# Optimization experiments

Measured on AMD Instinct MI355X. Metric: run time of the kernel, lower is better.

Reference implementation:

```python
import jax, jax.numpy as jnp
import numpy as np

N_NODES = 32768


def setup_inputs() -> dict:
    key = jax.random.key(0)
    ks = jax.random.split(key, 6)
    x = jax.random.normal(ks[0], (N_NODES, 128), dtype=jnp.float32)
    edge_index = jax.random.randint(ks[1], (2, 262144), 0, N_NODES, dtype=jnp.int64)
    weights = jax.random.normal(ks[2], (64, 128, 128), dtype=jnp.float32) * (1.0 / np.sqrt(128.0))
    biases = jax.random.normal(ks[3], (64, 128), dtype=jnp.float32) * 0.02
    cls_w = jax.random.normal(ks[4], (128, 4), dtype=jnp.float32) * (1.0 / np.sqrt(128.0))
    cls_b = jax.random.normal(ks[5], (4,), dtype=jnp.float32) * 0.02
    return {"x": x, "edge_index": edge_index, "weights": weights,
            "biases": biases, "cls_w": cls_w, "cls_b": cls_b}


def reference(x, edge_index, weights, biases, cls_w, cls_b):
    n = x.shape[0]
    # GCN normalization with self-loops (PyG GCNConv default):
    # A_hat = D^-1/2 (A + I) D^-1/2, deg counted on target nodes.
    loop = jnp.arange(n, dtype=edge_index.dtype)
    src = jnp.concatenate([edge_index[0], loop])  # [E+N]
    dst = jnp.concatenate([edge_index[1], loop])  # [E+N]
    deg = jax.ops.segment_sum(jnp.ones_like(dst, dtype=x.dtype), dst, num_segments=n)
    dinv = jnp.where(deg > 0, jax.lax.rsqrt(deg), 0.0)
    norm = dinv[src] * dinv[dst]  # [E+N]

    def gcn_layer(h, wb):
        W, b = wb
        hw = h @ W                                   # [N, H] dense transform
        msg = hw[src] * norm[:, None]                # gather + edge scaling
        agg = jax.ops.segment_sum(msg, dst, num_segments=n)  # scatter-add
        return jax.nn.relu(agg + b), None            # dropout is identity (eval)

    h, _ = jax.lax.scan(gcn_layer, x, (weights, biases))
    out = (h + x) @ cls_w + cls_b  # residual + linear classifier
    return out
```

## Files before the change

### kernel.cpp

```cpp
#include <hip/hip_runtime.h>
#include <hip/hip_bf16.h>

#define NN 32768
#define EE 262144
#define FD 128
#define NL 64
#define MROW 16
#define SROW 132

typedef short v8s __attribute__((ext_vector_type(8)));
typedef float v4f __attribute__((ext_vector_type(4)));

__device__ __forceinline__ unsigned short f2bf(float x) {
    unsigned u = __builtin_bit_cast(unsigned, x);
    u += 0x7fffu + ((u >> 16) & 1u);
    return (unsigned short)(u >> 16);
}
__device__ __forceinline__ float bf2f(unsigned short h) {
    unsigned u = ((unsigned)h) << 16;
    return __builtin_bit_cast(float, u);
}
__device__ __forceinline__ void acc8_bf16(float* acc, v8s r) {
    const int* d = (const int*)&r;
#pragma unroll
    for (int k = 0; k < 4; k++) {
        unsigned u = (unsigned)d[k];
        acc[2 * k]     += __builtin_bit_cast(float, u << 16);
        acc[2 * k + 1] += __builtin_bit_cast(float, u & 0xffff0000u);
    }
}

__global__ __launch_bounds__(256) void k_deg(const int* __restrict__ dst,
                                             int* __restrict__ cnt) {
    int e = blockIdx.x * 256 + threadIdx.x;
    if (e < EE) atomicAdd(&cnt[dst[e]], 1);
}

__global__ __launch_bounds__(256) void k_scanA(const int* __restrict__ cnt,
                                               int* __restrict__ bsum) {
    __shared__ int ws[4];
    int tid = threadIdx.x;
    int v = cnt[blockIdx.x * 256 + tid];
    int x = v;
#pragma unroll
    for (int off = 1; off < 64; off <<= 1) x += __shfl_xor(x, off);
    if ((tid & 63) == 0) ws[tid >> 6] = x;
    __syncthreads();
    if (tid == 0) bsum[blockIdx.x] = ws[0] + ws[1] + ws[2] + ws[3];
}
__global__ __launch_bounds__(128) void k_scanB(const int* __restrict__ bsum,
                                               int* __restrict__ boff,
                                               int* __restrict__ offs) {
    __shared__ int s0;
    int tid = threadIdx.x;
    int v = bsum[tid];
    int lane = tid & 63, w = tid >> 6;
    int x = v;
#pragma unroll
    for (int off = 1; off < 64; off <<= 1) {
        int y = __shfl_up(x, off);
        if (lane >= off) x += y;
    }
    if (tid == 63) s0 = x;
    __syncthreads();
    int excl = x - v + (w ? s0 : 0);
    boff[tid] = excl;
    if (tid == 127) offs[NN] = excl + v;
}
__global__ __launch_bounds__(256) void k_scanC(const int* __restrict__ cnt,
                                               const int* __restrict__ boff,
                                               int* __restrict__ offs,
                                               float* __restrict__ dinv) {
    __shared__ int ws[4];
    int tid = threadIdx.x;
    int i = blockIdx.x * 256 + tid;
    int v = cnt[i];
    int lane = tid & 63, w = tid >> 6;
    int x = v;
#pragma unroll
    for (int off = 1; off < 64; off <<= 1) {
        int y = __shfl_up(x, off);
        if (lane >= off) x += y;
    }
    if (lane == 63) ws[w] = x;
    __syncthreads();
    int wexcl = 0;
#pragma unroll
    for (int k = 0; k < 4; k++) if (k < w) wexcl += ws[k];
    offs[i] = boff[blockIdx.x] + wexcl + x - v;
    dinv[i] = rsqrtf((float)v + 1.0f);
}

__global__ __launch_bounds__(256) void k_prep(const int* __restrict__ src,
                                              const int* __restrict__ dst,
                                              const int* __restrict__ offs,
                                              int* __restrict__ cursor,
                                              int* __restrict__ col,
                                              const float* __restrict__ W,
                                              unsigned short* __restrict__ Whi,
                                              const float* __restrict__ x,
                                              const float* __restrict__ dinv,
                                              unsigned short* __restrict__ g) {
    int b = blockIdx.x;
    if (b < EE / 256) {
        int e = b * 256 + threadIdx.x;
        int s = src[e], d = dst[e];
        int slot = atomicAdd(&cursor[d], 1);
        col[offs[d] + slot] = s;
    } else if (b < EE / 256 + NL * 2048 / 256) {
        int t = (b - EE / 256) * 256 + threadIdx.x;
        int l = t >> 11;
        int rem = t & 2047;
        int ks = rem >> 9;
        int rem2 = rem & 511;
        int nt = rem2 >> 6;
        int L = rem2 & 63;
        const float* Wl = W + (size_t)l * FD * FD;
        int kbase = ks * 32 + ((L >> 4) << 3);
        int n = nt * 16 + (L & 15);
        v8s hv;
#pragma unroll
        for (int j = 0; j < 8; j++)
            hv[j] = (short)f2bf(Wl[(size_t)(kbase + j) * FD + n]);
        *(v8s*)(Whi + (size_t)t * 8) = hv;
    } else {
        int i = (b - EE / 256 - NL * 2048 / 256) * 256 + threadIdx.x;
        float di = dinv[(i * 8) >> 7];
        float4 a = *(const float4*)(x + (size_t)i * 8);
        float4 c = *(const float4*)(x + (size_t)i * 8 + 4);
        v8s o;
        o[0] = (short)f2bf(di * a.x); o[1] = (short)f2bf(di * a.y);
        o[2] = (short)f2bf(di * a.z); o[3] = (short)f2bf(di * a.w);
        o[4] = (short)f2bf(di * c.x); o[5] = (short)f2bf(di * c.y);
        o[6] = (short)f2bf(di * c.z); o[7] = (short)f2bf(di * c.w);
        *(v8s*)(g + (size_t)i * 8) = o;
    }
}

__global__ __launch_bounds__(256, 8) void k_layer(
        const unsigned short* __restrict__ g,
        const int* __restrict__ offs,
        const int* __restrict__ col,
        const unsigned short* __restrict__ Whi,
        const float* __restrict__ dinv,
        const float* __restrict__ bias,
        unsigned short* __restrict__ gout,
        const float* __restrict__ x,
        const float* __restrict__ cw,
        const float* __restrict__ cb,
        float* __restrict__ out,
        int last) {
    __shared__ unsigned short sA[MROW * SROW];
    __shared__ float sDinv[MROW];
    int tid = threadIdx.x;
    int lane = tid & 63;
    int w = tid >> 6;
    int row0 = blockIdx.x * MROW;
    int fg = lane >> 4;
    int fl = lane & 15;
    const unsigned short* gf = g + fl * 8;

    if (tid < MROW) sDinv[tid] = dinv[row0 + tid];

    int nbase = row0 + w * 4;
    int4 ov = *(const int4*)(offs + nbase);
    int o4 = offs[nbase + 4];
    int B0 = ov.x;
    int Etot = o4 - B0;

    if (Etot <= 64) {
        int c = (lane < Etot) ? col[B0 + lane] : 0;
        int node = nbase + fg;
        int sg = ((fg == 0) ? ov.x : (fg == 1) ? ov.y : (fg == 2) ? ov.z : ov.w) - B0;
        int eg = ((fg == 0) ? ov.y : (fg == 1) ? ov.z : (fg == 2) ? ov.w : o4) - B0;
        int len = eg - sg;
        int m = max(len, __shfl_xor(len, 16));
        m = max(m, __shfl_xor(m, 32));
        float acc[8];
#pragma unroll
        for (int k = 0; k < 8; k++) acc[k] = 0.f;
        for (int j = 0; j < m; j += 6) {
            int i0 = sg + j,     i1 = sg + j + 1, i2 = sg + j + 2;
            int i3 = sg + j + 3, i4 = sg + j + 4, i5 = sg + j + 5;
            bool p0 = i0 < eg, p1 = i1 < eg, p2 = i2 < eg;
            bool p3 = i3 < eg, p4 = i4 < eg, p5 = i5 < eg;
            int s0 = __shfl(c, i0 & 63);
            int s1 = __shfl(c, i1 & 63);
            int s2 = __shfl(c, i2 & 63);
            int s3 = __shfl(c, i3 & 63);
            int s4 = __shfl(c, i4 & 63);
            int s5 = __shfl(c, i5 & 63);
            v8s r0, r1, r2, r3, r4, r5;
            if (p0) r0 = *(const v8s*)(gf + (size_t)s0 * FD);
            if (p1) r1 = *(const v8s*)(gf + (size_t)s1 * FD);
            if (p2) r2 = *(const v8s*)(gf + (size_t)s2 * FD);
            if (p3) r3 = *(const v8s*)(gf + (size_t)s3 * FD);
            if (p4) r4 = *(const v8s*)(gf + (size_t)s4 * FD);
            if (p5) r5 = *(const v8s*)(gf + (size_t)s5 * FD);
            if (p0) acc8_bf16(acc, r0);
            if (p1) acc8_bf16(acc, r1);
            if (p2) acc8_bf16(acc, r2);
            if (p3) acc8_bf16(acc, r3);
            if (p4) acc8_bf16(acc, r4);
            if (p5) acc8_bf16(acc, r5);
        }
        v8s selfv = *(const v8s*)(gf + (size_t)node * FD);
        acc8_bf16(acc, selfv);
        float di = dinv[node];
        unsigned pk[4];
#pragma unroll
        for (int k = 0; k < 4; k++) {
            pk[k] = (unsigned)f2bf(di * acc[2 * k]) |
                    ((unsigned)f2bf(di * acc[2 * k + 1]) << 16);
        }
        *(v8s*)&sA[(w * 4 + fg) * SROW + fl * 8] = *(v8s*)pk;
    } else {
        for (int r = 0; r < 4; r++) {
            int nloc = w * 4 + r;
            int node = row0 + nloc;
            float acc[8];
#pragma unroll
            for (int k = 0; k < 8; k++) acc[k] = 0.f;
            int b = offs[node], e = offs[node + 1];
            int deg = e - b;
            for (int base = 0; base < deg; base += 64) {
                int n = min(deg - base, 64);
                int c = (lane < n) ? col[b + base + lane] : 0;
                for (int j = 0; j < n; j += 8) {
                    int e0 = j + fg, e1 = j + 4 + fg;
                    int s0 = __shfl(c, e0 & 63);
                    int s1 = __shfl(c, e1 & 63);
                    bool p0 = e0 < n, p1 = e1 < n;
                    v8s r0, r1;
                    if (p0) r0 = *(const v8s*)(gf + (size_t)s0 * FD);
                    if (p1) r1 = *(const v8s*)(gf + (size_t)s1 * FD);
                    if (p0) acc8_bf16(acc, r0);
                    if (p1) acc8_bf16(acc, r1);
                }
            }
#pragma unroll
            for (int k = 0; k < 8; k++) {
                acc[k] += __shfl_xor(acc[k], 16);
                acc[k] += __shfl_xor(acc[k], 32);
            }
            v8s sv = *(const v8s*)(gf + (size_t)node * FD);
            acc8_bf16(acc, sv);
            if (fg == 0) {
                float di = dinv[node];
                unsigned pk[4];
#pragma unroll
                for (int k = 0; k < 4; k++) {
                    pk[k] = (unsigned)f2bf(di * acc[2 * k]) |
                            ((unsigned)f2bf(di * acc[2 * k + 1]) << 16);
                }
                *(v8s*)&sA[nloc * SROW + fl * 8] = *(v8s*)pk;
            }
        }
    }
    __syncthreads();

    v4f a0 = (v4f){0.f, 0.f, 0.f, 0.f};
    v4f a1 = (v4f){0.f, 0.f, 0.f, 0.f};
#pragma unroll
    for (int ks = 0; ks < 4; ks++) {
        v8s ah = *(const v8s*)&sA[(lane & 15) * SROW + ks * 32 + ((lane >> 4) << 3)];
        size_t bo0 = ((size_t)(ks * 8 + w * 2) * 64 + lane) * 8;
        size_t bo1 = ((size_t)(ks * 8 + w * 2 + 1) * 64 + lane) * 8;
        v8s bh0 = *(const v8s*)(Whi + bo0);
        v8s bh1 = *(const v8s*)(Whi + bo1);
        a0 = __builtin_amdgcn_mfma_f32_16x16x32_bf16(ah, bh0, a0, 0, 0, 0);
        a1 = __builtin_amdgcn_mfma_f32_16x16x32_bf16(ah, bh1, a1, 0, 0, 0);
    }
    __syncthreads();

    float bb0 = bias[w * 32 + (lane & 15)];
    float bb1 = bias[w * 32 + 16 + (lane & 15)];
#pragma unroll
    for (int nt = 0; nt < 2; nt++) {
        int col_l = w * 32 + nt * 16 + (lane & 15);
        float bb = nt ? bb1 : bb0;
        v4f a = nt ? a1 : a0;
#pragma unroll
        for (int rg = 0; rg < 4; rg++) {
            int row_l = ((lane >> 4) << 2) + rg;
            float v = fmaxf(a[rg] + bb, 0.f);
            if (!last) v *= sDinv[row_l];
            sA[row_l * SROW + col_l] = f2bf(v);
        }
    }
    __syncthreads();

    if (!last) {
        int orow = tid >> 4;
        int ocol = (tid & 15) * 8;
        *(v8s*)(gout + (size_t)(row0 + orow) * FD + ocol) =
            *(const v8s*)&sA[orow * SROW + ocol];
    } else {
        int row = tid >> 4;
        int t = tid & 15;
        int nd = row0 + row;
        const unsigned short* hr = &sA[row * SROW + t * 8];
        const float* xr = x + (size_t)nd * FD + t * 8;
        float xv[8];
        *(float4*)&xv[0] = *(const float4*)xr;
        *(float4*)&xv[4] = *(const float4*)(xr + 4);
        float p0 = 0.f, p1 = 0.f, p2 = 0.f, p3 = 0.f;
#pragma unroll
        for (int j = 0; j < 8; j++) {
            float s = bf2f(hr[j]) + xv[j];
            float4 wv = *(const float4*)(cw + (size_t)(t * 8 + j) * 4);
            p0 += s * wv.x; p1 += s * wv.y; p2 += s * wv.z; p3 += s * wv.w;
        }
#pragma unroll
        for (int off = 1; off < 16; off <<= 1) {
            p0 += __shfl_xor(p0, off);
            p1 += __shfl_xor(p1, off);
            p2 += __shfl_xor(p2, off);
            p3 += __shfl_xor(p3, off);
        }
        if (t == 0) {
            float4 r = make_float4(p0 + cb[0], p1 + cb[1], p2 + cb[2], p3 + cb[3]);
            *(float4*)(out + (size_t)nd * 4) = r;
        }
    }
}

extern "C" void kernel_launch(void* const* d_in, const int* in_sizes, int n_in,
                              void* d_out, int out_size, void* d_ws, size_t ws_size,
                              hipStream_t stream) {
    const float* x       = (const float*)d_in[0];
    const int* ei        = (const int*)d_in[1];
    const float* weights = (const float*)d_in[2];
    const float* biases  = (const float*)d_in[3];
    const float* cls_w   = (const float*)d_in[4];
    const float* cls_b   = (const float*)d_in[5];
    float* out = (float*)d_out;

    char* ws = (char*)d_ws;
    size_t off = 0;
    auto alloc = [&](size_t bytes) -> void* {
        off = (off + 255) & ~(size_t)255;
        void* p = ws + off;
        off += bytes;
        return p;
    };
    int*   cnt    = (int*)alloc((size_t)NN * 4);
    int*   cursor = (int*)alloc((size_t)NN * 4);
    float* dinv   = (float*)alloc((size_t)NN * 4);
    int*   offs   = (int*)alloc((size_t)(NN + 1) * 4);
    int*   bsum   = (int*)alloc((size_t)128 * 4);
    int*   boff   = (int*)alloc((size_t)128 * 4);
    int*   col    = (int*)alloc((size_t)EE * 4);
    unsigned short* Whi = (unsigned short*)alloc((size_t)NL * FD * FD * 2);
    unsigned short* h0  = (unsigned short*)alloc((size_t)NN * FD * 2);
    unsigned short* h1  = (unsigned short*)alloc((size_t)NN * FD * 2);

    const int* srcv = ei;
    const int* dstv = ei + EE;

    hipMemsetAsync(cnt, 0, (size_t)NN * 4, stream);
    hipMemsetAsync(cursor, 0, (size_t)NN * 4, stream);
    k_deg<<<EE / 256, 256, 0, stream>>>(dstv, cnt);
    k_scanA<<<128, 256, 0, stream>>>(cnt, bsum);
    k_scanB<<<1, 128, 0, stream>>>(bsum, boff, offs);
    k_scanC<<<128, 256, 0, stream>>>(cnt, boff, offs, dinv);
    k_prep<<<EE / 256 + NL * 2048 / 256 + NN * FD / 2048, 256, 0, stream>>>(
        srcv, dstv, offs, cursor, col, weights, Whi, x, dinv, h1);

    const unsigned short* gin = h1;
    for (int l = 0; l < NL; l++) {
        unsigned short* gout = (l & 1) ? h1 : h0;
        k_layer<<<NN / MROW, 256, 0, stream>>>(gin, offs, col,
                                               Whi + (size_t)l * FD * FD,
                                               dinv, biases + (size_t)l * FD,
                                               gout, x, cls_w, cls_b, out,
                                               l == NL - 1);
        gin = gout;
    }
}
```

Baseline: 1.013 ms.

## Renumber nodes by in-degree bucket to balance per-block gather work

```diff
diff --git a/kernel.cpp b/kernel.cpp
--- a/kernel.cpp
+++ b/kernel.cpp
@@ -34,6 +34,40 @@
                                              int* __restrict__ cnt) {
     int e = blockIdx.x * 256 + threadIdx.x;
     if (e < EE) atomicAdd(&cnt[dst[e]], 1);
+}
+
+__global__ __launch_bounds__(256) void k_hist(const int* __restrict__ cnt,
+                                              int* __restrict__ hist) {
+    int i = blockIdx.x * 256 + threadIdx.x;
+    int d = cnt[i];
+    atomicAdd(&hist[d > 63 ? 63 : d], 1);
+}
+__global__ __launch_bounds__(64) void k_binscan(const int* __restrict__ hist,
+                                                int* __restrict__ hoff) {
+    int t = threadIdx.x;
+    int v = hist[t];
+    int x = v;
+#pragma unroll
+    for (int off = 1; off < 64; off <<= 1) {
+        int y = __shfl_up(x, off);
+        if (t >= off) x += y;
+    }
+    hoff[t] = x - v;
+}
+__global__ __launch_bounds__(256) void k_scatter(const int* __restrict__ cnt,
+                                                 const int* __restrict__ hoff,
+                                                 int* __restrict__ hcur,
+                                                 int* __restrict__ sortid,
+                                                 int* __restrict__ inv,
+                                                 int* __restrict__ cntS) {
+    int i = blockIdx.x * 256 + threadIdx.x;
+    int d = cnt[i];
+    int b = d > 63 ? 63 : d;
+    int r = atomicAdd(&hcur[b], 1);
+    int p = hoff[b] + r;
+    sortid[p] = i;
+    inv[i] = p;
+    cntS[p] = d;
 }
 
 __global__ __launch_bounds__(256) void k_scanA(const int* __restrict__ cnt,
@@ -93,6 +127,8 @@
 
 __global__ __launch_bounds__(256) void k_prep(const int* __restrict__ src,
                                               const int* __restrict__ dst,
+                                              const int* __restrict__ inv,
+                                              const int* __restrict__ sortid,
                                               const int* __restrict__ offs,
                                               int* __restrict__ cursor,
                                               int* __restrict__ col,
@@ -104,9 +140,10 @@
     int b = blockIdx.x;
     if (b < EE / 256) {
         int e = b * 256 + threadIdx.x;
-        int s = src[e], d = dst[e];
-        int slot = atomicAdd(&cursor[d], 1);
-        col[offs[d] + slot] = s;
+        int pd = inv[dst[e]];
+        int ps = inv[src[e]];
+        int slot = atomicAdd(&cursor[pd], 1);
+        col[offs[pd] + slot] = ps;
     } else if (b < EE / 256 + NL * 2048 / 256) {
         int t = (b - EE / 256) * 256 + threadIdx.x;
         int l = t >> 11;
@@ -125,15 +162,19 @@
         *(v8s*)(Whi + (size_t)t * 8) = hv;
     } else {
         int i = (b - EE / 256 - NL * 2048 / 256) * 256 + threadIdx.x;
-        float di = dinv[(i * 8) >> 7];
-        float4 a = *(const float4*)(x + (size_t)i * 8);
-        float4 c = *(const float4*)(x + (size_t)i * 8 + 4);
+        int p = i >> 4;
+        int ch = i & 15;
+        int orig = sortid[p];
+        float di = dinv[p];
+        const float* xr = x + (size_t)orig * FD + ch * 8;
+        float4 a = *(const float4*)xr;
+        float4 c = *(const float4*)(xr + 4);
         v8s o;
         o[0] = (short)f2bf(di * a.x); o[1] = (short)f2bf(di * a.y);
         o[2] = (short)f2bf(di * a.z); o[3] = (short)f2bf(di * a.w);
         o[4] = (short)f2bf(di * c.x); o[5] = (short)f2bf(di * c.y);
         o[6] = (short)f2bf(di * c.z); o[7] = (short)f2bf(di * c.w);
-        *(v8s*)(g + (size_t)i * 8) = o;
+        *(v8s*)(g + (size_t)p * FD + ch * 8) = o;
     }
 }
 
@@ -145,6 +186,7 @@
         const float* __restrict__ dinv,
         const float* __restrict__ bias,
         unsigned short* __restrict__ gout,
+        const int* __restrict__ sortid,
         const float* __restrict__ x,
         const float* __restrict__ cw,
         const float* __restrict__ cb,
@@ -298,9 +340,9 @@
     } else {
         int row = tid >> 4;
         int t = tid & 15;
-        int nd = row0 + row;
+        int orig = sortid[row0 + row];
         const unsigned short* hr = &sA[row * SROW + t * 8];
-        const float* xr = x + (size_t)nd * FD + t * 8;
+        const float* xr = x + (size_t)orig * FD + t * 8;
         float xv[8];
         *(float4*)&xv[0] = *(const float4*)xr;
         *(float4*)&xv[4] = *(const float4*)(xr + 4);
@@ -320,7 +362,7 @@
         }
         if (t == 0) {
             float4 r = make_float4(p0 + cb[0], p1 + cb[1], p2 + cb[2], p3 + cb[3]);
-            *(float4*)(out + (size_t)nd * 4) = r;
+            *(float4*)(out + (size_t)orig * 4) = r;
         }
     }
 }
@@ -350,6 +392,11 @@
     int*   offs   = (int*)alloc((size_t)(NN + 1) * 4);
     int*   bsum   = (int*)alloc((size_t)128 * 4);
     int*   boff   = (int*)alloc((size_t)128 * 4);
+    int*   hist   = (int*)alloc((size_t)128 * 4);
+    int*   hoff   = (int*)alloc((size_t)64 * 4);
+    int*   sortid = (int*)alloc((size_t)NN * 4);
+    int*   inv    = (int*)alloc((size_t)NN * 4);
+    int*   cntS   = (int*)alloc((size_t)NN * 4);
     int*   col    = (int*)alloc((size_t)EE * 4);
     unsigned short* Whi = (unsigned short*)alloc((size_t)NL * FD * FD * 2);
     unsigned short* h0  = (unsigned short*)alloc((size_t)NN * FD * 2);
@@ -360,12 +407,18 @@
 
     hipMemsetAsync(cnt, 0, (size_t)NN * 4, stream);
     hipMemsetAsync(cursor, 0, (size_t)NN * 4, stream);
+    hipMemsetAsync(hist, 0, (size_t)128 * 4, stream);
     k_deg<<<EE / 256, 256, 0, stream>>>(dstv, cnt);
-    k_scanA<<<128, 256, 0, stream>>>(cnt, bsum);
+    k_hist<<<NN / 256, 256, 0, stream>>>(cnt, hist);
+    k_binscan<<<1, 64, 0, stream>>>(hist, hoff);
+    k_scatter<<<NN / 256, 256, 0, stream>>>(cnt, hoff, hist + 64,
+                                            sortid, inv, cntS);
+    k_scanA<<<128, 256, 0, stream>>>(cntS, bsum);
     k_scanB<<<1, 128, 0, stream>>>(bsum, boff, offs);
-    k_scanC<<<128, 256, 0, stream>>>(cnt, boff, offs, dinv);
+    k_scanC<<<128, 256, 0, stream>>>(cntS, boff, offs, dinv);
     k_prep<<<EE / 256 + NL * 2048 / 256 + NN * FD / 2048, 256, 0, stream>>>(
-        srcv, dstv, offs, cursor, col, weights, Whi, x, dinv, h1);
+        srcv, dstv, inv, sortid, offs, cursor, col,
+        weights, Whi, x, dinv, h1);
 
     const unsigned short* gin = h1;
     for (int l = 0; l < NL; l++) {
@@ -373,8 +426,8 @@
         k_layer<<<NN / MROW, 256, 0, stream>>>(gin, offs, col,
                                                Whi + (size_t)l * FD * FD,
                                                dinv, biases + (size_t)l * FD,
-                                               gout, x, cls_w, cls_b, out,
-                                               l == NL - 1);
+                                               gout, sortid, x, cls_w, cls_b,
+                                               out, l == NL - 1);
         gin = gout;
     }
 }
```

Measured after the change: 1.566 ms. 54.5% more time.
